# Kernel tuning notes

Measured on AMD Instinct MI355X. Metric: run time of the kernel, lower is better.

The kernel has to match this reference:

```python
import jax, jax.numpy as jnp
import numpy as np

ALPHA = 0.2  # leaky relu slope
NEG_BIG = -9e15


def setup_inputs() -> dict:
    key = jax.random.key(0)
    k1, k2, k3, k4 = jax.random.split(key, 4)
    B, N, Fin, Fout = 8, 2048, 128, 128
    h = jax.random.normal(k1, (B, N, Fin), dtype=jnp.float32)
    adj = jax.random.randint(k2, (N, N), 0, 2, dtype=jnp.int32)
    # xavier_uniform with gain=1.414
    limW = 1.414 * np.sqrt(6.0 / (Fin + Fout))
    W = jax.random.uniform(k3, (Fin, Fout), minval=-limW, maxval=limW, dtype=jnp.float32)
    lima = 1.414 * np.sqrt(6.0 / (2 * Fout + 1))
    a = jax.random.uniform(k4, (2 * Fout, 1), minval=-lima, maxval=lima, dtype=jnp.float32)
    return {"h": h, "adj": adj, "W": W, "a": a}


def reference(h, adj, W, a):
    # Wh: [B, N, F]
    Wh = jnp.einsum("bnf,fo->bno", h, W)
    Fout = W.shape[1]
    a1, a2 = a[:Fout, 0], a[Fout:, 0]  # [F], [F]
    # Additive score decomposition (same math as concat trick):
    # e[b,i,j] = leakyrelu(Wh_i . a1 + Wh_j . a2)
    s1 = Wh @ a1  # [B, N] (source/query part)
    s2 = Wh @ a2  # [B, N] (target part)
    e = s1[:, :, None] + s2[:, None, :]  # [B, N, N]
    e = jnp.where(e > 0, e, ALPHA * e)   # leaky relu
    e = jnp.where(adj[None, :, :] > 0, e, NEG_BIG)
    attention = jax.nn.softmax(e, axis=2)  # [B, N, N]
    # dropout is identity in eval mode
    h_prime = jnp.einsum("bij,bjf->bif", attention, Wh)
    return h_prime
```

## Files before the change

### kernel.cpp

```cpp
#include <hip/hip_runtime.h>
#include <hip/hip_bf16.h>
#include <stdint.h>

#define ALPHA 0.2f

typedef __attribute__((ext_vector_type(8))) short bf16x8;
typedef __attribute__((ext_vector_type(4))) float f32x4;

__device__ __forceinline__ short f2bf(float f) {
    union { float f; uint32_t u; } c; c.f = f;
    uint32_t u = c.u + 0x7FFF + ((c.u >> 16) & 1);
    return (short)(u >> 16);
}

__device__ __forceinline__ uint32_t pk_bf16(float lo, float hi) {
    union { float f; uint32_t u; } a, b;
    a.f = lo; b.f = hi;
    return __builtin_amdgcn_perm(b.u + 0x8000u, a.u + 0x8000u, 0x07060302u);
}

__global__ __launch_bounds__(256) void pack_adj_kernel(
        const int* __restrict__ adj, uint8_t* __restrict__ bytes,
        const float* __restrict__ W, short* __restrict__ WTg) {
    int t = blockIdx.x * 256 + threadIdx.x;
    const int4* a4 = reinterpret_cast<const int4*>(adj) + (size_t)t * 2;
    int4 x0 = a4[0], x1 = a4[1];
    uint32_t m = 0;
    m |= (x0.x > 0) ? 1u   : 0u;  m |= (x0.y > 0) ? 2u   : 0u;
    m |= (x0.z > 0) ? 4u   : 0u;  m |= (x0.w > 0) ? 8u   : 0u;
    m |= (x1.x > 0) ? 16u  : 0u;  m |= (x1.y > 0) ? 32u  : 0u;
    m |= (x1.z > 0) ? 64u  : 0u;  m |= (x1.w > 0) ? 128u : 0u;
    bytes[t] = (uint8_t)m;

    if (blockIdx.x < 64) {
        int idx = blockIdx.x * 256 + threadIdx.x;
        int k = idx >> 7, f = idx & 127;
        WTg[f * 128 + k] = f2bf(W[k * 128 + f]);
    }
}

__global__ __launch_bounds__(256) void wh_kernel(
        const float* __restrict__ h, const short* __restrict__ WTg,
        const float* __restrict__ a, short* __restrict__ whT,
        float* __restrict__ s1g, float* __restrict__ s2g) {
    __shared__ float sred[4][2][16];
    __shared__ short tr[4][32][24];

    int tid = threadIdx.x, wid = tid >> 6, lane = tid & 63;
    int q = lane >> 4, n = lane & 15;
    int bb = blockIdx.x & 7;
    int tile = blockIdx.x >> 3;
    int rb = bb * 2048 + tile * 16;
    int row = rb + n;

    f32x4 acc[2] = {};
    #pragma unroll
    for (int kc = 0; kc < 4; ++kc) {
        const float* hp = h + (size_t)row * 128 + kc * 32 + q * 8;
        float4 h0 = reinterpret_cast<const float4*>(hp)[0];
        float4 h1 = reinterpret_cast<const float4*>(hp)[1];
        bf16x8 afrag;
        afrag[0] = f2bf(h0.x); afrag[1] = f2bf(h0.y);
        afrag[2] = f2bf(h0.z); afrag[3] = f2bf(h0.w);
        afrag[4] = f2bf(h1.x); afrag[5] = f2bf(h1.y);
        afrag[6] = f2bf(h1.z); afrag[7] = f2bf(h1.w);
        #pragma unroll
        for (int u = 0; u < 2; ++u) {
            int t = wid * 2 + u;
            bf16x8 bfrag = *reinterpret_cast<const bf16x8*>(
                WTg + (t * 16 + n) * 128 + kc * 32 + q * 8);
            acc[u] = __builtin_amdgcn_mfma_f32_16x16x32_bf16(afrag, bfrag, acc[u], 0, 0, 0);
        }
    }

    float p1[4] = {0.f, 0.f, 0.f, 0.f}, p2[4] = {0.f, 0.f, 0.f, 0.f};
    #pragma unroll
    for (int u = 0; u < 2; ++u) {
        int c = (wid * 2 + u) * 16 + n;
        float a1c = a[c], a2c = a[128 + c];
        #pragma unroll
        for (int r = 0; r < 4; ++r) {
            p1[r] += acc[u][r] * a1c;
            p2[r] += acc[u][r] * a2c;
        }
    }
    #pragma unroll
    for (int d = 1; d < 16; d <<= 1) {
        #pragma unroll
        for (int r = 0; r < 4; ++r) {
            p1[r] += __shfl_xor(p1[r], d);
            p2[r] += __shfl_xor(p2[r], d);
        }
    }
    if (n == 0) {
        #pragma unroll
        for (int r = 0; r < 4; ++r) {
            sred[wid][0][q * 4 + r] = p1[r];
            sred[wid][1][q * 4 + r] = p2[r];
        }
    }

    #pragma unroll
    for (int u = 0; u < 2; ++u)
        #pragma unroll
        for (int r = 0; r < 4; ++r)
            tr[wid][u * 16 + n][q * 4 + r] = f2bf(acc[u][r]);
    __syncthreads();

    if (wid == 0 && lane < 16) {
        float v1 = 0.f, v2 = 0.f;
        #pragma unroll
        for (int v = 0; v < 4; ++v) { v1 += sred[v][0][lane]; v2 += sred[v][1][lane]; }
        s1g[rb + lane] = v1;
        s2g[rb + lane] = v2;
    }

    int jr = rb & 2047;
    int fl = lane & 31, jh = lane >> 5;
    bf16x8 v = *reinterpret_cast<const bf16x8*>(&tr[wid][fl][jh * 8]);
    int f = wid * 32 + fl;
    int jc = jr >> 5, jo = (jr & 31) + jh * 8;
    *reinterpret_cast<bf16x8*>(
        whT + ((size_t)(bb * 64 + jc) * 128 + f) * 32 + jo) = v;
}

__global__ __launch_bounds__(256, 4) void attn_kernel(
        const short* __restrict__ whT, const float* __restrict__ s1g,
        const float* __restrict__ s2g, const uint8_t* __restrict__ adjb,
        float* __restrict__ out) {
    __shared__ f32x4 buf[4][8][64];
    __shared__ float lds_ds[4][16];

    int wid = threadIdx.x >> 6, lane = threadIdx.x & 63;
    int q = lane >> 4, n = lane & 15;
    int b  = blockIdx.x & 7;
    int ib = (blockIdx.x >> 3) * 16;
    int rowA = ib + n;

    float s1A = s1g[b * 2048 + rowA];
    const float* s2b = s2g + b * 2048;
    int jbase = wid * 512;

    uint4 mregA = *reinterpret_cast<const uint4*>(
        adjb + (size_t)rowA * 256 + wid * 64 + q * 16);
    const uint32_t* mrA = reinterpret_cast<const uint32_t*>(&mregA);

    float4 s2va = *reinterpret_cast<const float4*>(s2b + jbase + lane * 8);
    float4 s2vb = *reinterpret_cast<const float4*>(s2b + jbase + lane * 8 + 4);
    float s2v[8] = {s2va.x, s2va.y, s2va.z, s2va.w,
                    s2vb.x, s2vb.y, s2vb.z, s2vb.w};

    const short* bpn = whT + (size_t)b * 262144 + n * 32 + q * 8;

    f32x4 accA[8] = {};
    float dsA = 0.f;

    bf16x8 nb[2][8];
    {
        const short* bp = bpn + (size_t)(jbase >> 5) * 4096;
        #pragma unroll
        for (int t = 0; t < 8; ++t)
            nb[0][t] = *reinterpret_cast<const bf16x8*>(bp + t * 512);
    }

    #pragma unroll
    for (int c = 0; c < 16; ++c) {
        const int cur = c & 1, nxt = cur ^ 1;
        int k1 = jbase + ((c + 1) & 15) * 32;
        const short* bp = bpn + (size_t)(k1 >> 5) * 4096;
        #pragma unroll
        for (int t = 0; t < 8; ++t)
            nb[nxt][t] = *reinterpret_cast<const bf16x8*>(bp + t * 512);

        int srcl = (c >> 2) * 16 + n;
        uint32_t mA = ((uint32_t)__shfl((int)mrA[c & 3], srcl)) >> (q * 8);

        int s2src = c * 4 + q;
        float s2arr[8];
        #pragma unroll
        for (int j = 0; j < 8; ++j) s2arr[j] = __shfl(s2v[j], s2src);

        float pA[8];
        #pragma unroll
        for (int j = 0; j < 8; ++j) {
            float eA = s1A + s2arr[j];
            eA = fmaxf(eA, ALPHA * eA);
            float vA = ((mA >> j) & 1) ? __expf(eA) : 0.0f;
            dsA += vA; pA[j] = vA;
        }
        union { uint32_t u[4]; bf16x8 v; } cvA;
        #pragma unroll
        for (int p = 0; p < 4; ++p)
            cvA.u[p] = pk_bf16(pA[2 * p], pA[2 * p + 1]);

        #pragma unroll
        for (int t = 0; t < 8; ++t)
            accA[t] = __builtin_amdgcn_mfma_f32_16x16x32_bf16(cvA.v, nb[cur][t], accA[t], 0, 0, 0);
    }

    dsA += __shfl_xor(dsA, 16); dsA += __shfl_xor(dsA, 32);
    if (q == 0) lds_ds[wid][n] = dsA;

    #pragma unroll
    for (int i = 0; i < 8; ++i) buf[wid][i][lane] = accA[i];
    __syncthreads();

    int t0 = wid * 2, t1 = wid * 2 + 1;
    f32x4 rA0 = buf[0][t0][lane] + buf[1][t0][lane] + buf[2][t0][lane] + buf[3][t0][lane];
    f32x4 rA1 = buf[0][t1][lane] + buf[1][t1][lane] + buf[2][t1][lane] + buf[3][t1][lane];

    float dAt = lds_ds[0][n] + lds_ds[1][n] + lds_ds[2][n] + lds_ds[3][n];
    float rdA[4];
    #pragma unroll
    for (int r = 0; r < 4; ++r)
        rdA[r] = 1.0f / __shfl(dAt, q * 4 + r);

    size_t ob = ((size_t)b * 2048 + ib) * 128;
    #pragma unroll
    for (int r = 0; r < 4; ++r) {
        out[ob + (size_t)(q * 4 + r) * 128 + t0 * 16 + n] = rA0[r] * rdA[r];
        out[ob + (size_t)(q * 4 + r) * 128 + t1 * 16 + n] = rA1[r] * rdA[r];
    }
}

extern "C" void kernel_launch(void* const* d_in, const int* in_sizes, int n_in,
                              void* d_out, int out_size, void* d_ws, size_t ws_size,
                              hipStream_t stream) {
    const float* h   = (const float*)d_in[0];
    const int*   adj = (const int*)d_in[1];
    const float* W   = (const float*)d_in[2];
    const float* a   = (const float*)d_in[3];
    float* out = (float*)d_out;

    char* ws = (char*)d_ws;
    short* whT = (short*)ws;
    float* s1  = (float*)(ws + 4194304);
    float* s2  = (float*)(ws + 4259840);
    uint8_t* bytes = (uint8_t*)(ws + 4325376);

    short* WTg = (short*)d_out + (4194304 - 16384);

    pack_adj_kernel<<<2048, 256, 0, stream>>>(adj, bytes, W, WTg);
    wh_kernel<<<1024, 256, 0, stream>>>(h, WTg, a, whT, s1, s2);
    attn_kernel<<<1024, 256, 0, stream>>>(whT, s1, s2, bytes, out);
}
```

Baseline: 121.4 us.

## Share Wh tiles across four row-groups via double-buffered LDS async loads

The attention kernel now processes 64 query rows per block, one 16-row group per wave, with each wave covering all 2048 columns. Previously the four waves split the column range and reduced partial results through LDS. Wh tiles are streamed into a double-buffered 64KB LDS region with global_load_lds and shared by all four waves. The whT layout written by wh_kernel changes so the LDS reads come out lane-contiguous. This cuts redundant global reads of Wh and removes the cross-wave reduction, at the cost of 4x fewer blocks (256) and a barrier per stage, which may reduce occupancy and latency hiding.

Result: faster. 114.6 us (-5.6%).

```diff
diff --git a/kernel.cpp b/kernel.cpp
--- a/kernel.cpp
+++ b/kernel.cpp
@@ -17,6 +17,12 @@
     union { float f; uint32_t u; } a, b;
     a.f = lo; b.f = hi;
     return __builtin_amdgcn_perm(b.u + 0x8000u, a.u + 0x8000u, 0x07060302u);
+}
+
+__device__ __forceinline__ void gload_lds16(const void* g, void* l) {
+    __builtin_amdgcn_global_load_lds(
+        (const __attribute__((address_space(1))) void*)g,
+        (__attribute__((address_space(3))) void*)l, 16, 0, 0);
 }
 
 __global__ __launch_bounds__(256) void pack_adj_kernel(
@@ -119,108 +125,111 @@
     int fl = lane & 31, jh = lane >> 5;
     bf16x8 v = *reinterpret_cast<const bf16x8*>(&tr[wid][fl][jh * 8]);
     int f = wid * 32 + fl;
-    int jc = jr >> 5, jo = (jr & 31) + jh * 8;
+    int t = f >> 4, nn = f & 15;
+    int jc = jr >> 5;
+    int qg = ((jr & 31) >> 3) + jh;
     *reinterpret_cast<bf16x8*>(
-        whT + ((size_t)(bb * 64 + jc) * 128 + f) * 32 + jo) = v;
-}
-
-__global__ __launch_bounds__(256, 4) void attn_kernel(
+        whT + (size_t)(bb * 64 + jc) * 4096 + t * 512 + qg * 128 + nn * 8) = v;
+}
+
+__global__ __launch_bounds__(256) void attn_kernel(
         const short* __restrict__ whT, const float* __restrict__ s1g,
         const float* __restrict__ s2g, const uint8_t* __restrict__ adjb,
         float* __restrict__ out) {
-    __shared__ f32x4 buf[4][8][64];
-    __shared__ float lds_ds[4][16];
+    __shared__ char sbuf[2][32768];
 
     int wid = threadIdx.x >> 6, lane = threadIdx.x & 63;
     int q = lane >> 4, n = lane & 15;
     int b  = blockIdx.x & 7;
-    int ib = (blockIdx.x >> 3) * 16;
-    int rowA = ib + n;
+    int ib = (blockIdx.x >> 3) * 64;
+    int rowA = ib + wid * 16 + n;
 
     float s1A = s1g[b * 2048 + rowA];
     const float* s2b = s2g + b * 2048;
-    int jbase = wid * 512;
-
-    uint4 mregA = *reinterpret_cast<const uint4*>(
-        adjb + (size_t)rowA * 256 + wid * 64 + q * 16);
-    const uint32_t* mrA = reinterpret_cast<const uint32_t*>(&mregA);
-
-    float4 s2va = *reinterpret_cast<const float4*>(s2b + jbase + lane * 8);
-    float4 s2vb = *reinterpret_cast<const float4*>(s2b + jbase + lane * 8 + 4);
-    float s2v[8] = {s2va.x, s2va.y, s2va.z, s2va.w,
-                    s2vb.x, s2vb.y, s2vb.z, s2vb.w};
-
-    const short* bpn = whT + (size_t)b * 262144 + n * 32 + q * 8;
-
-    f32x4 accA[8] = {};
-    float dsA = 0.f;
-
-    bf16x8 nb[2][8];
+    const uint32_t* admA = reinterpret_cast<const uint32_t*>(
+        adjb + (size_t)rowA * 256);
+    const char* gbase = reinterpret_cast<const char*>(whT) + (size_t)b * 524288;
+
+    f32x4 acc[8] = {};
+    float ds = 0.f;
+
+    uint32_t mw[4];
+    float4 s2l[4], s2h[4];
+    #pragma unroll
+    for (int u = 0; u < 4; ++u) {
+        mw[u] = admA[u];
+        s2l[u] = *reinterpret_cast<const float4*>(s2b + u * 32 + q * 8);
+        s2h[u] = *reinterpret_cast<const float4*>(s2b + u * 32 + q * 8 + 4);
+    }
+
     {
-        const short* bp = bpn + (size_t)(jbase >> 5) * 4096;
-        #pragma unroll
-        for (int t = 0; t < 8; ++t)
-            nb[0][t] = *reinterpret_cast<const bf16x8*>(bp + t * 512);
-    }
-
-    #pragma unroll
-    for (int c = 0; c < 16; ++c) {
-        const int cur = c & 1, nxt = cur ^ 1;
-        int k1 = jbase + ((c + 1) & 15) * 32;
-        const short* bp = bpn + (size_t)(k1 >> 5) * 4096;
-        #pragma unroll
-        for (int t = 0; t < 8; ++t)
-            nb[nxt][t] = *reinterpret_cast<const bf16x8*>(bp + t * 512);
-
-        int srcl = (c >> 2) * 16 + n;
-        uint32_t mA = ((uint32_t)__shfl((int)mrA[c & 3], srcl)) >> (q * 8);
-
-        int s2src = c * 4 + q;
-        float s2arr[8];
-        #pragma unroll
-        for (int j = 0; j < 8; ++j) s2arr[j] = __shfl(s2v[j], s2src);
-
-        float pA[8];
-        #pragma unroll
-        for (int j = 0; j < 8; ++j) {
-            float eA = s1A + s2arr[j];
-            eA = fmaxf(eA, ALPHA * eA);
-            float vA = ((mA >> j) & 1) ? __expf(eA) : 0.0f;
-            dsA += vA; pA[j] = vA;
-        }
-        union { uint32_t u[4]; bf16x8 v; } cvA;
-        #pragma unroll
-        for (int p = 0; p < 4; ++p)
-            cvA.u[p] = pk_bf16(pA[2 * p], pA[2 * p + 1]);
-
-        #pragma unroll
-        for (int t = 0; t < 8; ++t)
-            accA[t] = __builtin_amdgcn_mfma_f32_16x16x32_bf16(cvA.v, nb[cur][t], accA[t], 0, 0, 0);
-    }
-
-    dsA += __shfl_xor(dsA, 16); dsA += __shfl_xor(dsA, 32);
-    if (q == 0) lds_ds[wid][n] = dsA;
-
-    #pragma unroll
-    for (int i = 0; i < 8; ++i) buf[wid][i][lane] = accA[i];
+        const char* g = gbase + wid * 8192 + lane * 16;
+        char* l = &sbuf[0][wid * 8192];
+        #pragma unroll
+        for (int i = 0; i < 8; ++i)
+            gload_lds16(g + i * 1024, l + i * 1024);
+    }
     __syncthreads();
 
-    int t0 = wid * 2, t1 = wid * 2 + 1;
-    f32x4 rA0 = buf[0][t0][lane] + buf[1][t0][lane] + buf[2][t0][lane] + buf[3][t0][lane];
-    f32x4 rA1 = buf[0][t1][lane] + buf[1][t1][lane] + buf[2][t1][lane] + buf[3][t1][lane];
-
-    float dAt = lds_ds[0][n] + lds_ds[1][n] + lds_ds[2][n] + lds_ds[3][n];
-    float rdA[4];
-    #pragma unroll
-    for (int r = 0; r < 4; ++r)
-        rdA[r] = 1.0f / __shfl(dAt, q * 4 + r);
-
-    size_t ob = ((size_t)b * 2048 + ib) * 128;
-    #pragma unroll
-    for (int r = 0; r < 4; ++r) {
-        out[ob + (size_t)(q * 4 + r) * 128 + t0 * 16 + n] = rA0[r] * rdA[r];
-        out[ob + (size_t)(q * 4 + r) * 128 + t1 * 16 + n] = rA1[r] * rdA[r];
-    }
+    for (int s = 0; s < 16; ++s) {
+        int cur = s & 1;
+        if (s < 15) {
+            const char* g = gbase + (size_t)(s + 1) * 32768 + wid * 8192 + lane * 16;
+            char* l = &sbuf[cur ^ 1][wid * 8192];
+            #pragma unroll
+            for (int i = 0; i < 8; ++i)
+                gload_lds16(g + i * 1024, l + i * 1024);
+        }
+        const char* lb = sbuf[cur];
+        #pragma unroll
+        for (int u = 0; u < 4; ++u) {
+            int c = s * 4 + u;
+            bf16x8 nb[8];
+            const char* cb = lb + u * 8192 + lane * 16;
+            #pragma unroll
+            for (int t = 0; t < 8; ++t)
+                nb[t] = *reinterpret_cast<const bf16x8*>(cb + t * 1024);
+
+            uint32_t mA = mw[u] >> (q * 8);
+            float s2arr[8] = {s2l[u].x, s2l[u].y, s2l[u].z, s2l[u].w,
+                              s2h[u].x, s2h[u].y, s2h[u].z, s2h[u].w};
+
+            int cn = c + 4; if (cn > 63) cn = 63;
+            mw[u] = admA[cn];
+            s2l[u] = *reinterpret_cast<const float4*>(s2b + cn * 32 + q * 8);
+            s2h[u] = *reinterpret_cast<const float4*>(s2b + cn * 32 + q * 8 + 4);
+
+            float p[8];
+            #pragma unroll
+            for (int j = 0; j < 8; ++j) {
+                float e = s1A + s2arr[j];
+                e = fmaxf(e, ALPHA * e);
+                float v = ((mA >> j) & 1) ? __expf(e) : 0.0f;
+                ds += v; p[j] = v;
+            }
+            union { uint32_t u32[4]; bf16x8 v; } cv;
+            #pragma unroll
+            for (int pp = 0; pp < 4; ++pp)
+                cv.u32[pp] = pk_bf16(p[2 * pp], p[2 * pp + 1]);
+
+            #pragma unroll
+            for (int t = 0; t < 8; ++t)
+                acc[t] = __builtin_amdgcn_mfma_f32_16x16x32_bf16(cv.v, nb[t], acc[t], 0, 0, 0);
+        }
+        __syncthreads();
+    }
+
+    ds += __shfl_xor(ds, 16); ds += __shfl_xor(ds, 32);
+    float rd[4];
+    #pragma unroll
+    for (int r = 0; r < 4; ++r) rd[r] = 1.0f / __shfl(ds, q * 4 + r);
+
+    size_t ob = ((size_t)b * 2048 + ib + wid * 16) * 128;
+    #pragma unroll
+    for (int t = 0; t < 8; ++t)
+        #pragma unroll
+        for (int r = 0; r < 4; ++r)
+            out[ob + (size_t)(q * 4 + r) * 128 + t * 16 + n] = acc[t][r] * rd[r];
 }
 
 extern "C" void kernel_launch(void* const* d_in, const int* in_sizes, int n_in,
@@ -242,5 +251,5 @@
 
     pack_adj_kernel<<<2048, 256, 0, stream>>>(adj, bytes, W, WTg);
     wh_kernel<<<1024, 256, 0, stream>>>(h, WTg, a, whT, s1, s2);
-    attn_kernel<<<1024, 256, 0, stream>>>(whT, s1, s2, bytes, out);
-}
+    attn_kernel<<<256, 256, 0, stream>>>(whT, s1, s2, bytes, out);
+}
```
